# Kernel tuning notes

Measured on AMD Instinct MI355X. Metric: run time of the kernel, lower is better.

Reference implementation:

```python
import jax, jax.numpy as jnp
import numpy as np

D = 4          # subsample stride for quantized refs
R = 6          # local search radius
P = 2 * R + 1  # 13
N = P * P      # 169
C = 32         # one-hot classes
BETA = 50.0
SIG = 1.0      # gaussian kernel sigma for kernel_soft_argmax
MPR = 12       # memory_patch_R
MPP = 2 * MPR + 1  # 25
DIL_INT = 15


def bilinear_gather(img, ys, xs):
    # img (b,c,h,w); ys,xs (b,n,h,w) float pixel coords; zero padding outside.
    b, c, h, w = img.shape
    y0f = jnp.floor(ys); x0f = jnp.floor(xs)
    wy = ys - y0f; wx = xs - x0f
    y0 = y0f.astype(jnp.int32); x0 = x0f.astype(jnp.int32)
    imgf = img.reshape(b, c, h * w)

    def corner(yi, xi, wgt):
        valid = (yi >= 0) & (yi < h) & (xi >= 0) & (xi < w)
        idx = jnp.clip(yi, 0, h - 1) * w + jnp.clip(xi, 0, w - 1)  # (b,n,h,w)
        g = jax.vmap(lambda f, ix: f[:, ix])(imgf, idx)            # (b,c,n,h,w)
        return g * (wgt * valid)[:, None]

    return (corner(y0, x0, (1 - wy) * (1 - wx))
            + corner(y0, x0 + 1, (1 - wy) * wx)
            + corner(y0 + 1, x0, wy * (1 - wx))
            + corner(y0 + 1, x0 + 1, wy * wx))


def deform_im2col(img, offset):
    # img (b,c,h,w); offset (b,h,w,2) ordered (dx,dy); returns (b,c,N,h,w)
    b, c, h, w = img.shape
    n = jnp.arange(N)
    dy = (n // P - R).astype(jnp.float32)
    dx = (n % P - R).astype(jnp.float32)
    yy = jnp.arange(h, dtype=jnp.float32)[:, None]
    xx = jnp.arange(w, dtype=jnp.float32)[None, :]
    ys = yy[None, None] + offset[..., 1][:, None] + dy[None, :, None, None]
    xs = xx[None, None] + offset[..., 0][:, None] + dx[None, :, None, None]
    return bilinear_gather(img, ys, xs)


def local_corr(t, r, rad, dil):
    # SpatialCorrelationSampler(kernel_size=1, patch_size=2*rad+1, dilation_patch=dil)
    pad = rad * dil
    rp = jnp.pad(r, ((0, 0), (0, 0), (pad, pad), (pad, pad)))
    offs = jnp.arange(2 * rad + 1) * dil

    def dot(oy, ox):
        rs = jax.lax.dynamic_slice(rp, (0, 0, oy, ox), t.shape)
        return jnp.sum(t * rs, axis=1)  # (b,h,w)

    f = jax.vmap(lambda oy: jax.vmap(lambda ox: dot(oy, ox))(offs))(offs)  # (Pp,Pp,b,h,w)
    return jnp.transpose(f, (2, 0, 1, 3, 4))  # (b,Pp,Pp,h,w), axis1=dy, axis2=dx


def unfold(x, ksz, pad):
    # torch F.unfold: (b,c,h,w) -> (b,c,ksz*ksz,h*w), n = ky*ksz+kx, zero pad
    b, c, h, w = x.shape
    xp = jnp.pad(x, ((0, 0), (0, 0), (pad, pad), (pad, pad)))
    offs = jnp.arange(ksz)
    sl = jax.vmap(lambda oy: jax.vmap(
        lambda ox: jax.lax.dynamic_slice(xp, (0, 0, oy, ox), x.shape))(offs))(offs)
    return jnp.transpose(sl, (2, 3, 0, 1, 4, 5)).reshape(b, c, ksz * ksz, h * w)


def kernel_soft_argmax(corr):
    # corr (B, N, h, w): gaussian-weight then softmax(beta * .) over N
    k = jnp.arange(P, dtype=jnp.float32)
    ctr = (P - 1) / 2.0
    g = jnp.exp(-(((k[None, :] - ctr) ** 2) + ((k[:, None] - ctr) ** 2)) / (2 * SIG ** 2))
    return jax.nn.softmax(BETA * (g.reshape(1, N, 1, 1) * corr), axis=1)


def get_grid(corr):
    # corr (B, N, h, w) -> soft-argmax grid (B, h, w, 2) in normalized coords
    B, n, h, w = corr.shape
    # replicate the torch meshgrid variable swap in the original get_grid
    x_map = jnp.broadcast_to(jnp.linspace(-1.0, 1.0, w)[None, :], (h, w)).astype(jnp.float32)
    y_map = jnp.broadcast_to(jnp.linspace(-1.0, 1.0, h)[:, None], (h, w)).astype(jnp.float32)
    xg = unfold(x_map[None, None], P, R)[:, 0]  # (1,N,hw)
    yg = unfold(y_map[None, None], P, R)[:, 0]
    wgt = corr.reshape(B, n, h * w)
    wgt = wgt / jnp.sum(wgt, 1, keepdims=True)
    gx = (wgt * xg).sum(1).reshape(B, h, w, 1)
    gy = (wgt * yg).sum(1).reshape(B, h, w, 1)
    return jnp.concatenate([gx, gy], 3)


def forward(feats_r, feats_t, quantized_r, ref_index, current_ind):
    ref_list = [int(v) for v in np.asarray(ref_index)]  # static config
    cur = int(current_ind)
    nref = feats_r.shape[0]
    nsearch = len([x for x in ref_list if cur - x > DIL_INT])
    dirates = [min(4, (cur - x) // DIL_INT + 1) for x in ref_list if cur - x > DIL_INT]
    b, c, h, w = feats_t.shape

    mdy = jnp.arange(-MPR, MPR + 1, dtype=jnp.float32)
    corrs, offsets = [], []
    for si in range(nsearch):
        cc = local_corr(feats_t, feats_r[si], MPR, dirates[si])       # (b,25,25,h,w)
        cc = jax.nn.softmax(cc.reshape(b, MPP * MPP, h * w), axis=1)
        cc = cc.reshape(b, MPP, MPP, h, w)
        offx = jnp.einsum('bpqhw,q->bhw', cc, mdy)   # expectation of dx
        offy = jnp.einsum('bpqhw,p->bhw', cc, mdy)   # expectation of dy
        off = jnp.stack([offx, offy], -1) * float(dirates[si])        # (b,h,w,2)
        offsets.append(off)
        col0 = deform_im2col(feats_r[si], off)                        # (b,c,N,h,w)
        corrs.append(jnp.einsum('bchw,bcnhw->bnhw', feats_t, col0))
    for ind in range(nsearch, nref):
        corrs.append(local_corr(feats_t, feats_r[ind], R, 1).reshape(b, N, h, w))

    corr = jnp.concatenate(corrs, 0)                 # (b*nref, N, h, w)
    corr = kernel_soft_argmax(corr)
    corr = corr.reshape(b, 1, N * nref, h * w)
    grid = get_grid(corr.reshape(-1, N, h, w))       # (b*nref, h, w, 2)

    # prep: subsample ::D and one-hot single-channel label maps
    labels = quantized_r[:, :, 0, ::D, ::D]          # (nref, b, h, w)
    qr = (labels[:, :, None] == jnp.arange(C)[None, None, :, None, None]).astype(jnp.float32)

    cols = []
    for i in range(nsearch):
        cols.append(deform_im2col(qr[i], offsets[i]).reshape(b, C, N, h * w))
    for i in range(nsearch, nref):
        cols.append(unfold(qr[i], P, R))
    image_uf = jnp.concatenate(cols, 2)              # (b, C, N*nref, hw)

    out = jnp.einsum('bnl,bcnl->bcl', corr[:, 0], image_uf).reshape(b, C, h, w)
    return out, grid


def setup_inputs() -> dict:
    key = jax.random.key(0)
    k1, k2, k3 = jax.random.split(key, 3)
    feats_r = jax.random.normal(k1, (3, 1, 64, 64, 64), dtype=jnp.float32)
    feats_t = jax.random.normal(k2, (1, 64, 64, 64), dtype=jnp.float32)
    quantized_r = jax.random.randint(k3, (3, 1, 1, 256, 256), 0, C, dtype=jnp.int32)
    return {
        'feats_r': feats_r,
        'feats_t': feats_t,
        'quantized_r': quantized_r,
        'ref_index': np.arange(3),
        'current_ind': 16,
    }


def reference(feats_r, feats_t, quantized_r, ref_index, current_ind):
    return forward(feats_r, feats_t, quantized_r, ref_index, current_ind)
```

## Files before the change

kernel.cpp:

```cpp
#include <hip/hip_runtime.h>


#define NPIX 4096

__device__ __forceinline__ float pdot(float4 t0, float4 t1, float4 t2,
                                      float4 t3, float4 a, float4 b, float4 c,
                                      float4 d) {
  float s0 = 0.f, s1 = 0.f, s2 = 0.f, s3 = 0.f;
  s0 = fmaf(t0.x, a.x, s0); s1 = fmaf(t0.y, a.y, s1);
  s2 = fmaf(t0.z, a.z, s2); s3 = fmaf(t0.w, a.w, s3);
  s0 = fmaf(t1.x, b.x, s0); s1 = fmaf(t1.y, b.y, s1);
  s2 = fmaf(t1.z, b.z, s2); s3 = fmaf(t1.w, b.w, s3);
  s0 = fmaf(t2.x, c.x, s0); s1 = fmaf(t2.y, c.y, s1);
  s2 = fmaf(t2.z, c.z, s2); s3 = fmaf(t2.w, c.w, s3);
  s0 = fmaf(t3.x, d.x, s0); s1 = fmaf(t3.y, d.y, s1);
  s2 = fmaf(t3.z, d.z, s2); s3 = fmaf(t3.w, d.w, s3);
  return (s0 + s1) + (s2 + s3);
}

__device__ __forceinline__ float qdot(float4 ta, float4 tb, float4 tc,
                                      float4 td,
                                      const float* __restrict__ rbase,
                                      int tx) {
  const float4* r = (const float4*)rbase;
  float v = pdot(ta, tb, tc, td, r[tx], r[tx + 4], r[tx + 8], r[tx + 12]);
  v += __shfl_xor(v, 1);
  v += __shfl_xor(v, 2);
  return v;
}

__device__ __forceinline__ float xpose_reduce4(float p0, float p1, float p2,
                                               float p3, int tx) {
  bool o1 = tx & 1, o2 = tx & 2;
  float x01 = __shfl_xor(o1 ? p0 : p1, 1);
  float x23 = __shfl_xor(o1 ? p2 : p3, 1);
  float sA = (o1 ? p1 : p0) + x01;
  float sB = (o1 ? p3 : p2) + x23;
  float z = __shfl_xor(o2 ? sA : sB, 2);
  return o2 ? (sB + z) : (sA + z);
}

__global__ __launch_bounds__(256) void k_transpose(
    const float* __restrict__ ft, const float* __restrict__ fr,
    float* __restrict__ tT, float* __restrict__ rT) {
  __shared__ float tile[64][65];
  int img = blockIdx.y;
  int pixBase = blockIdx.x * 64;
  const float* src = (img == 0) ? ft : fr + (img - 1) * (64 * NPIX);
  float* dst = (img == 0) ? tT : rT + (img - 1) * (64 * NPIX);
  int tid = threadIdx.x;
#pragma unroll
  for (int it = 0; it < 16; ++it) {
    int li = it * 256 + tid;
    int c = li >> 6, p = li & 63;
    tile[p][c] = src[c * NPIX + pixBase + p];
  }
  __syncthreads();
#pragma unroll
  for (int it = 0; it < 16; ++it) {
    int li = it * 256 + tid;
    int p = li >> 6, c = li & 63;
    dst[(pixBase + p) * 64 + c] = tile[p][c];
  }
}

#define LOADT(N, XC)                                                       \
  const float4* tp##N = (const float4*)&tT[((y << 6) + (XC)) << 6];        \
  float4 t##N##0 = tp##N[tx], t##N##1 = tp##N[tx + 4],                     \
         t##N##2 = tp##N[tx + 8], t##N##3 = tp##N[tx + 12];

__global__ __launch_bounds__(256) void k_corr_all(
    const float* __restrict__ tT, const float* __restrict__ rT,
    float* __restrict__ off, float* __restrict__ corrws,
    float* __restrict__ grid) {
  int z = blockIdx.z;
  int xg = blockIdx.x, y = blockIdx.y;
  int tid = threadIdx.x;
  int g = tid >> 2, tx = tid & 3;
  int w = tid >> 6, lane = tid & 63;
  __shared__ float cc[4][625];
  __shared__ float offs[4][2];

  if (z == 0) {
    int x0 = (xg >> 1) * 8 + (xg & 1);
    LOADT(0, x0 + 0) LOADT(1, x0 + 2) LOADT(2, x0 + 4) LOADT(3, x0 + 6)

#pragma unroll 2
    for (int r = 0; r < 11; ++r) {
      int tu = g + (r << 6);
      if (tu < 700) {
        int oy = tu / 28, u = tu - oy * 28;
        int ry = y + 2 * (oy - 12), rx = x0 - 24 + 2 * u;
        float4 ra, rb, rc, rd;
        if ((unsigned)ry < 64u && (unsigned)rx < 64u) {
          const float4* rp = (const float4*)&rT[(ry * 64 + rx) * 64];
          ra = rp[tx]; rb = rp[tx + 4]; rc = rp[tx + 8]; rd = rp[tx + 12];
        } else {
          ra = rb = rc = rd = make_float4(0.f, 0.f, 0.f, 0.f);
        }
        float p0 = pdot(t00, t01, t02, t03, ra, rb, rc, rd);
        float p1 = pdot(t10, t11, t12, t13, ra, rb, rc, rd);
        float p2 = pdot(t20, t21, t22, t23, ra, rb, rc, rd);
        float p3 = pdot(t30, t31, t32, t33, ra, rb, rc, rd);
        float v = xpose_reduce4(p0, p1, p2, p3, tx);
        int ox = u - tx;
        if ((unsigned)ox < 25u) cc[tx][oy * 25 + ox] = v;
      }
    }
    __syncthreads();

    {
      float vv[10];
      float lmax = -3e38f;
#pragma unroll
      for (int it = 0; it < 10; ++it) {
        int o = lane + it * 64;
        float v = (o < 625) ? cc[w][o] : -3e38f;
        vv[it] = v;
        lmax = fmaxf(lmax, v);
      }
#pragma unroll
      for (int o = 32; o; o >>= 1) lmax = fmaxf(lmax, __shfl_down(lmax, o));
      float m = __shfl(lmax, 0);
      float s = 0.f, sx = 0.f, sy = 0.f;
#pragma unroll
      for (int it = 0; it < 10; ++it) {
        int o = lane + it * 64;
        int oy = o / 25, ox = o - oy * 25;
        float e = __expf(vv[it] - m);
        s += e;
        sx += e * (float)(ox - 12);
        sy += e * (float)(oy - 12);
      }
#pragma unroll
      for (int o = 32; o; o >>= 1) {
        s += __shfl_down(s, o);
        sx += __shfl_down(sx, o);
        sy += __shfl_down(sy, o);
      }
      if (lane == 0) {
        float ox_ = 2.f * sx / s, oy_ = 2.f * sy / s;
        offs[w][0] = ox_;
        offs[w][1] = oy_;
        int pix = y * 64 + x0 + 2 * w;
        off[pix * 2 + 0] = ox_;
        off[pix * 2 + 1] = oy_;
      }
    }
    __syncthreads();

    float(*D)[196] = (float(*)[196]) & cc[0][0];
#pragma unroll 1
    for (int r = 0; r < 13; ++r) {
      int s3 = g + (r << 6);
      if (s3 < 784) {
        int p = s3 / 196;
        int idx = s3 - p * 196;
        int a = idx / 14, b2 = idx - a * 14;
        float offx = offs[p][0], offy = offs[p][1];
        int px = x0 + 2 * p;
        int iy0 = y + (int)floorf(offy), ix0 = px + (int)floorf(offx);
        int ry = iy0 - 6 + a, rx = ix0 - 6 + b2;
        float v = 0.f;
        if ((unsigned)ry < 64u && (unsigned)rx < 64u) {
          const float4* tq = (const float4*)&tT[(y * 64 + px) * 64];
          v = qdot(tq[tx], tq[tx + 4], tq[tx + 8], tq[tx + 12],
                   &rT[(ry * 64 + rx) * 64], tx);
        }
        if (tx == 0) D[p][idx] = v;
      }
    }
    __syncthreads();

    {
      int px = x0 + 2 * w;
      int pix = y * 64 + px;
      float offx = offs[w][0], offy = offs[w][1];
      float fy = floorf(offy), fx = floorf(offx);
      float wy = offy - fy, wx = offx - fx;
      float w00 = (1.f - wy) * (1.f - wx), w01 = (1.f - wy) * wx;
      float w10 = wy * (1.f - wx), w11 = wy * wx;
      float sc[3];
      float lmax = -3e38f;
#pragma unroll
      for (int it = 0; it < 3; ++it) {
        int o = lane + it * 64;
        float scv = -3e38f;
        if (o < 169) {
          int i = o / 13, j = o - i * 13;
          float v = w00 * D[w][i * 14 + j] + w01 * D[w][i * 14 + j + 1] +
                    w10 * D[w][(i + 1) * 14 + j] +
                    w11 * D[w][(i + 1) * 14 + j + 1];
          float di = (float)((i - 6) * (i - 6) + (j - 6) * (j - 6));
          scv = 50.f * __expf(-0.5f * di) * v;
        }
        sc[it] = scv;
        lmax = fmaxf(lmax, scv);
      }
#pragma unroll
      for (int o = 32; o; o >>= 1) lmax = fmaxf(lmax, __shfl_down(lmax, o));
      float m = __shfl(lmax, 0);
      float ee[3];
      float s = 0.f, gx = 0.f, gy = 0.f;
#pragma unroll
      for (int it = 0; it < 3; ++it) {
        int o = lane + it * 64;
        int i = o / 13, j = o - i * 13;
        float e = __expf(sc[it] - m);
        ee[it] = e;
        int yy = y + i - 6, xx = px + j - 6;
        bool inb = (o < 169) && (unsigned)yy < 64u && (unsigned)xx < 64u;
        float xgv = inb ? (-1.f + (2.f / 63.f) * (float)xx) : 0.f;
        float ygv = inb ? (-1.f + (2.f / 63.f) * (float)yy) : 0.f;
        s += e;
        gx += e * xgv;
        gy += e * ygv;
      }
#pragma unroll
      for (int o = 32; o; o >>= 1) {
        s += __shfl_down(s, o);
        gx += __shfl_down(gx, o);
        gy += __shfl_down(gy, o);
      }
      float S = __shfl(s, 0);
#pragma unroll
      for (int it = 0; it < 3; ++it) {
        int o = lane + it * 64;
        if (o < 169) corrws[pix * 169 + o] = ee[it] / S;
      }
      if (lane == 0) {
        grid[pix * 2 + 0] = gx / S;
        grid[pix * 2 + 1] = gy / S;
      }
    }
  } else {
    int k = z;
    int x0 = xg * 4;
    const float* rb0 = rT + k * (64 * NPIX);
    LOADT(0, x0 + 0) LOADT(1, x0 + 1) LOADT(2, x0 + 2) LOADT(3, x0 + 3)
    float(*cc2)[169] = (float(*)[169]) & cc[0][0];

#pragma unroll 2
    for (int r = 0; r < 4; ++r) {
      int tu = g + (r << 6);
      if (tu < 208) {
        int i = tu >> 4, u = tu & 15;
        int ry = y + i - 6, rx = x0 - 6 + u;
        float4 ra, rbv, rc, rd;
        if ((unsigned)ry < 64u && (unsigned)rx < 64u) {
          const float4* rp = (const float4*)&rb0[(ry * 64 + rx) * 64];
          ra = rp[tx]; rbv = rp[tx + 4]; rc = rp[tx + 8]; rd = rp[tx + 12];
        } else {
          ra = rbv = rc = rd = make_float4(0.f, 0.f, 0.f, 0.f);
        }
        float p0 = pdot(t00, t01, t02, t03, ra, rbv, rc, rd);
        float p1 = pdot(t10, t11, t12, t13, ra, rbv, rc, rd);
        float p2 = pdot(t20, t21, t22, t23, ra, rbv, rc, rd);
        float p3 = pdot(t30, t31, t32, t33, ra, rbv, rc, rd);
        float v = xpose_reduce4(p0, p1, p2, p3, tx);
        int j = u - tx;
        if ((unsigned)j < 13u) cc2[tx][i * 13 + j] = v;
      }
    }
    __syncthreads();

    int px = x0 + w;
    int pix = y * 64 + px;
    float sc[3];
    float lmax = -3e38f;
#pragma unroll
    for (int it = 0; it < 3; ++it) {
      int o = lane + it * 64;
      float scv = -3e38f;
      if (o < 169) {
        int i = o / 13, j = o - i * 13;
        float di = (float)((i - 6) * (i - 6) + (j - 6) * (j - 6));
        scv = 50.f * __expf(-0.5f * di) * cc2[w][o];
      }
      sc[it] = scv;
      lmax = fmaxf(lmax, scv);
    }
#pragma unroll
    for (int o = 32; o; o >>= 1) lmax = fmaxf(lmax, __shfl_down(lmax, o));
    float m = __shfl(lmax, 0);
    float ee[3];
    float s = 0.f, gx = 0.f, gy = 0.f;
#pragma unroll
    for (int it = 0; it < 3; ++it) {
      int o = lane + it * 64;
      int i = o / 13, j = o - i * 13;
      float e = __expf(sc[it] - m);
      ee[it] = e;
      int yy = y + i - 6, xx = px + j - 6;
      bool inb = (o < 169) && (unsigned)yy < 64u && (unsigned)xx < 64u;
      float xgv = inb ? (-1.f + (2.f / 63.f) * (float)xx) : 0.f;
      float ygv = inb ? (-1.f + (2.f / 63.f) * (float)yy) : 0.f;
      s += e;
      gx += e * xgv;
      gy += e * ygv;
    }
#pragma unroll
    for (int o = 32; o; o >>= 1) {
      s += __shfl_down(s, o);
      gx += __shfl_down(gx, o);
      gy += __shfl_down(gy, o);
    }
    float S = __shfl(s, 0);
#pragma unroll
    for (int it = 0; it < 3; ++it) {
      int o = lane + it * 64;
      if (o < 169) corrws[(k * NPIX + pix) * 169 + o] = ee[it] / S;
    }
    if (lane == 0) {
      grid[(k * NPIX + pix) * 2 + 0] = gx / S;
      grid[(k * NPIX + pix) * 2 + 1] = gy / S;
    }
  }
}

__global__ __launch_bounds__(256) void k_out(const float* __restrict__ corrws,
                                             const float* __restrict__ off,
                                             const int* __restrict__ q,
                                             float* __restrict__ out) {
  int tid = threadIdx.x;
  int pix0 = blockIdx.x * 8;
  __shared__ float bins[8][32];
  __shared__ float cr[8][169];
  __shared__ float offs[8][2];
  bins[tid >> 5][tid & 31] = 0.f;
  if (tid < 16) offs[tid >> 1][tid & 1] = off[(pix0 + (tid >> 1)) * 2 + (tid & 1)];
  for (int i = tid; i < 8 * 169; i += 256) {
    int g = i / 169, n = i - g * 169;
    cr[g][n] = corrws[(pix0 + g) * 169 + n];
  }
  __syncthreads();

  for (int s = tid; s < 8 * 196; s += 256) {
    int g = s / 196, m = s - g * 196;
    int a = m / 14, b = m - a * 14;
    int pix = pix0 + g, y = pix >> 6, x = pix & 63;
    float offx = offs[g][0], offy = offs[g][1];
    float fy = floorf(offy), fx = floorf(offx);
    float wy = offy - fy, wx = offx - fx;
    int ry = y + (int)fy - 6 + a, rx = x + (int)fx - 6 + b;
    if ((unsigned)ry < 64u && (unsigned)rx < 64u) {
      float w00 = (1.f - wy) * (1.f - wx), w01 = (1.f - wy) * wx;
      float w10 = wy * (1.f - wx), w11 = wy * wx;
      float wgt = 0.f;
      if (a < 13) {
        if (b < 13) wgt = fmaf(w00, cr[g][a * 13 + b], wgt);
        if (b > 0) wgt = fmaf(w01, cr[g][a * 13 + b - 1], wgt);
      }
      if (a > 0) {
        if (b < 13) wgt = fmaf(w10, cr[g][(a - 1) * 13 + b], wgt);
        if (b > 0) wgt = fmaf(w11, cr[g][(a - 1) * 13 + b - 1], wgt);
      }
      if (wgt != 0.f) {
        int lbl = q[ry * 1024 + rx * 4];
        atomicAdd(&bins[g][lbl], wgt);
      }
    }
  }

  for (int k = 1; k < 3; ++k) {
    __syncthreads();
    for (int i = tid; i < 8 * 169; i += 256) {
      int g = i / 169, n = i - g * 169;
      cr[g][n] = corrws[((k << 12) + pix0 + g) * 169 + n];
    }
    __syncthreads();
    for (int s = tid; s < 8 * 169; s += 256) {
      int g = s / 169, n = s - g * 169;
      int i2 = n / 13, j2 = n - i2 * 13;
      int pix = pix0 + g, y = pix >> 6, x = pix & 63;
      int yy = y + i2 - 6, xx = x + j2 - 6;
      if ((unsigned)yy < 64u && (unsigned)xx < 64u) {
        int lbl = q[k * 65536 + yy * 1024 + xx * 4];
        atomicAdd(&bins[g][lbl], cr[g][n]);
      }
    }
  }
  __syncthreads();
  out[(tid >> 3) * NPIX + pix0 + (tid & 7)] = bins[tid & 7][tid >> 3];
}

extern "C" void kernel_launch(void* const* d_in, const int* in_sizes, int n_in,
                              void* d_out, int out_size, void* d_ws,
                              size_t ws_size, hipStream_t stream) {
  const float* fr = (const float*)d_in[0];
  const float* ft = (const float*)d_in[1];
  const int* q = (const int*)d_in[2];
  float* out = (float*)d_out;
  float* grid = out + 32 * NPIX;

  float* ws = (float*)d_ws;
  float* tT = ws;
  float* rT = ws + 262144;
  float* off = ws + 1048576;
  float* corrws = ws + 1056768;

  k_transpose<<<dim3(64, 4), 256, 0, stream>>>(ft, fr, tT, rT);
  k_corr_all<<<dim3(16, 64, 3), 256, 0, stream>>>(tT, rT, off, corrws, grid);
  k_out<<<512, 256, 0, stream>>>(corrws, off, q, out);
}
```

Before: 61.44 us.

## Pack subsampled labels to bytes, restructure correlation loops with clamped branchless loads

The transpose kernel now also writes the subsampled labels as a compact byte array. k_out copies all three reference label planes into shared memory and maps threads to a fixed 2D (a,b) window per pixel, which removes divisions and strided global label reads. The correlation phases replace divide/modulo indexing and per-thread branches with fixed row/column assignments, clamped loads and masked results. Phase 3 reuses the target registers already loaded instead of reloading them. Each k_out block now loads 12KB of labels, which adds redundant traffic and shared-memory pressure.

```diff
diff --git a/kernel.cpp b/kernel.cpp
--- a/kernel.cpp
+++ b/kernel.cpp
@@ -18,17 +18,6 @@
   return (s0 + s1) + (s2 + s3);
 }
 
-__device__ __forceinline__ float qdot(float4 ta, float4 tb, float4 tc,
-                                      float4 td,
-                                      const float* __restrict__ rbase,
-                                      int tx) {
-  const float4* r = (const float4*)rbase;
-  float v = pdot(ta, tb, tc, td, r[tx], r[tx + 4], r[tx + 8], r[tx + 12]);
-  v += __shfl_xor(v, 1);
-  v += __shfl_xor(v, 2);
-  return v;
-}
-
 __device__ __forceinline__ float xpose_reduce4(float p0, float p1, float p2,
                                                float p3, int tx) {
   bool o1 = tx & 1, o2 = tx & 2;
@@ -42,7 +31,8 @@
 
 __global__ __launch_bounds__(256) void k_transpose(
     const float* __restrict__ ft, const float* __restrict__ fr,
-    float* __restrict__ tT, float* __restrict__ rT) {
+    const int* __restrict__ q, float* __restrict__ tT, float* __restrict__ rT,
+    unsigned char* __restrict__ lblp) {
   __shared__ float tile[64][65];
   int img = blockIdx.y;
   int pixBase = blockIdx.x * 64;
@@ -62,12 +52,37 @@
     int p = li >> 6, c = li & 63;
     dst[(pixBase + p) * 64 + c] = tile[p][c];
   }
+  if (img >= 1 && tid < 64) {
+    int pix = pixBase + tid;
+    lblp[(img - 1) * 4096 + pix] =
+        (unsigned char)q[(img - 1) * 65536 + (pix >> 6) * 1024 + (pix & 63) * 4];
+  }
 }
 
 #define LOADT(N, XC)                                                       \
   const float4* tp##N = (const float4*)&tT[((y << 6) + (XC)) << 6];        \
   float4 t##N##0 = tp##N[tx], t##N##1 = tp##N[tx + 4],                     \
          t##N##2 = tp##N[tx + 8], t##N##3 = tp##N[tx + 12];
+
+__device__ __forceinline__ void phase3_px(
+    float4 T0, float4 T1, float4 T2, float4 T3, int iy0, int ix0,
+    const float* __restrict__ rT, float* __restrict__ Dp, int aB, int b3,
+    int tx) {
+#pragma unroll 1
+  for (int r = 0; r < 4; ++r) {
+    int a = aB + 4 * r;
+    int ry = iy0 + a, rx = ix0 + b3;
+    bool ok = (a < 14) & (b3 < 14) & ((unsigned)ry < 64u) & ((unsigned)rx < 64u);
+    int ryc = min(max(ry, 0), 63), rxc = min(max(rx, 0), 63);
+    const float4* rp = (const float4*)&rT[(ryc * 64 + rxc) * 64 + tx * 4];
+    float4 ra = rp[0], rb = rp[4], rc = rp[8], rd = rp[12];
+    float v = pdot(T0, T1, T2, T3, ra, rb, rc, rd);
+    v += __shfl_xor(v, 1);
+    v += __shfl_xor(v, 2);
+    v = ok ? v : 0.f;
+    if ((a < 14) && (b3 < 14) && tx == 0) Dp[a * 14 + b3] = v;
+  }
+}
 
 __global__ __launch_bounds__(256) void k_corr_all(
     const float* __restrict__ tT, const float* __restrict__ rT,
@@ -85,26 +100,32 @@
     int x0 = (xg >> 1) * 8 + (xg & 1);
     LOADT(0, x0 + 0) LOADT(1, x0 + 2) LOADT(2, x0 + 4) LOADT(3, x0 + 6)
 
-#pragma unroll 2
-    for (int r = 0; r < 11; ++r) {
-      int tu = g + (r << 6);
-      if (tu < 700) {
-        int oy = tu / 28, u = tu - oy * 28;
-        int ry = y + 2 * (oy - 12), rx = x0 - 24 + 2 * u;
-        float4 ra, rb, rc, rd;
-        if ((unsigned)ry < 64u && (unsigned)rx < 64u) {
-          const float4* rp = (const float4*)&rT[(ry * 64 + rx) * 64];
-          ra = rp[tx]; rb = rp[tx + 4]; rc = rp[tx + 8]; rd = rp[tx + 12];
-        } else {
-          ra = rb = rc = rd = make_float4(0.f, 0.f, 0.f, 0.f);
-        }
+    {
+      int u = g & 31;
+      int rx = x0 - 24 + 2 * u;
+      bool col_ok = ((unsigned)rx < 64u) & (u < 28);
+      int rx_c = min(max(rx, 0), 63);
+      int colB = rx_c * 64 + tx * 4;
+      int ox = u - tx;
+      bool st_col = (unsigned)ox < 25u;
+      int oy = g >> 5;
+      int ry = y + 2 * oy - 24;
+#pragma unroll 1
+      for (int r = 0; r < 13; ++r) {
+        bool oy_ok = oy < 25;
+        bool ok = col_ok & oy_ok & ((unsigned)ry < 64u);
+        int ry_c = min(max(ry, 0), 63);
+        const float4* rp = (const float4*)&rT[ry_c * 4096 + colB];
+        float4 ra = rp[0], rb = rp[4], rc = rp[8], rd = rp[12];
         float p0 = pdot(t00, t01, t02, t03, ra, rb, rc, rd);
         float p1 = pdot(t10, t11, t12, t13, ra, rb, rc, rd);
         float p2 = pdot(t20, t21, t22, t23, ra, rb, rc, rd);
         float p3 = pdot(t30, t31, t32, t33, ra, rb, rc, rd);
         float v = xpose_reduce4(p0, p1, p2, p3, tx);
-        int ox = u - tx;
-        if ((unsigned)ox < 25u) cc[tx][oy * 25 + ox] = v;
+        v = ok ? v : 0.f;
+        if (st_col && oy_ok) cc[tx][oy * 25 + ox] = v;
+        oy += 2;
+        ry += 4;
       }
     }
     __syncthreads();
@@ -150,24 +171,27 @@
     __syncthreads();
 
     float(*D)[196] = (float(*)[196]) & cc[0][0];
-#pragma unroll 1
-    for (int r = 0; r < 13; ++r) {
-      int s3 = g + (r << 6);
-      if (s3 < 784) {
-        int p = s3 / 196;
-        int idx = s3 - p * 196;
-        int a = idx / 14, b2 = idx - a * 14;
-        float offx = offs[p][0], offy = offs[p][1];
-        int px = x0 + 2 * p;
-        int iy0 = y + (int)floorf(offy), ix0 = px + (int)floorf(offx);
-        int ry = iy0 - 6 + a, rx = ix0 - 6 + b2;
-        float v = 0.f;
-        if ((unsigned)ry < 64u && (unsigned)rx < 64u) {
-          const float4* tq = (const float4*)&tT[(y * 64 + px) * 64];
-          v = qdot(tq[tx], tq[tx + 4], tq[tx + 8], tq[tx + 12],
-                   &rT[(ry * 64 + rx) * 64], tx);
-        }
-        if (tx == 0) D[p][idx] = v;
+    {
+      int b3 = g & 15, aB = g >> 4;
+      {
+        float offx = offs[0][0], offy = offs[0][1];
+        phase3_px(t00, t01, t02, t03, y + (int)floorf(offy) - 6,
+                  x0 + 0 + (int)floorf(offx) - 6, rT, &D[0][0], aB, b3, tx);
+      }
+      {
+        float offx = offs[1][0], offy = offs[1][1];
+        phase3_px(t10, t11, t12, t13, y + (int)floorf(offy) - 6,
+                  x0 + 2 + (int)floorf(offx) - 6, rT, &D[1][0], aB, b3, tx);
+      }
+      {
+        float offx = offs[2][0], offy = offs[2][1];
+        phase3_px(t20, t21, t22, t23, y + (int)floorf(offy) - 6,
+                  x0 + 4 + (int)floorf(offx) - 6, rT, &D[2][0], aB, b3, tx);
+      }
+      {
+        float offx = offs[3][0], offy = offs[3][1];
+        phase3_px(t30, t31, t32, t33, y + (int)floorf(offy) - 6,
+                  x0 + 6 + (int)floorf(offx) - 6, rT, &D[3][0], aB, b3, tx);
       }
     }
     __syncthreads();
@@ -240,26 +264,32 @@
     LOADT(0, x0 + 0) LOADT(1, x0 + 1) LOADT(2, x0 + 2) LOADT(3, x0 + 3)
     float(*cc2)[169] = (float(*)[169]) & cc[0][0];
 
-#pragma unroll 2
-    for (int r = 0; r < 4; ++r) {
-      int tu = g + (r << 6);
-      if (tu < 208) {
-        int i = tu >> 4, u = tu & 15;
-        int ry = y + i - 6, rx = x0 - 6 + u;
-        float4 ra, rbv, rc, rd;
-        if ((unsigned)ry < 64u && (unsigned)rx < 64u) {
-          const float4* rp = (const float4*)&rb0[(ry * 64 + rx) * 64];
-          ra = rp[tx]; rbv = rp[tx + 4]; rc = rp[tx + 8]; rd = rp[tx + 12];
-        } else {
-          ra = rbv = rc = rd = make_float4(0.f, 0.f, 0.f, 0.f);
-        }
+    {
+      int u2 = g & 15;
+      int rx = x0 - 6 + u2;
+      bool col_ok = (unsigned)rx < 64u;
+      int rx_c = min(max(rx, 0), 63);
+      int colB = rx_c * 64 + tx * 4;
+      int j = u2 - tx;
+      bool st_col = (unsigned)j < 13u;
+      int i = g >> 4;
+      int ry = y + i - 6;
+#pragma unroll 1
+      for (int r = 0; r < 4; ++r) {
+        bool i_ok = i < 13;
+        bool ok = col_ok & i_ok & ((unsigned)ry < 64u);
+        int ry_c = min(max(ry, 0), 63);
+        const float4* rp = (const float4*)&rb0[ry_c * 4096 + colB];
+        float4 ra = rp[0], rbv = rp[4], rc = rp[8], rd = rp[12];
         float p0 = pdot(t00, t01, t02, t03, ra, rbv, rc, rd);
         float p1 = pdot(t10, t11, t12, t13, ra, rbv, rc, rd);
         float p2 = pdot(t20, t21, t22, t23, ra, rbv, rc, rd);
         float p3 = pdot(t30, t31, t32, t33, ra, rbv, rc, rd);
         float v = xpose_reduce4(p0, p1, p2, p3, tx);
-        int j = u - tx;
-        if ((unsigned)j < 13u) cc2[tx][i * 13 + j] = v;
+        v = ok ? v : 0.f;
+        if (st_col && i_ok) cc2[tx][i * 13 + j] = v;
+        i += 4;
+        ry += 4;
       }
     }
     __syncthreads();
@@ -318,65 +348,81 @@
   }
 }
 
-__global__ __launch_bounds__(256) void k_out(const float* __restrict__ corrws,
-                                             const float* __restrict__ off,
-                                             const int* __restrict__ q,
-                                             float* __restrict__ out) {
+__global__ __launch_bounds__(256) void k_out(
+    const float* __restrict__ corrws, const float* __restrict__ off,
+    const unsigned char* __restrict__ lblp, float* __restrict__ out) {
   int tid = threadIdx.x;
   int pix0 = blockIdx.x * 8;
-  __shared__ float bins[8][32];
+  __shared__ float bins[8][33];
   __shared__ float cr[8][169];
-  __shared__ float offs[8][2];
-  bins[tid >> 5][tid & 31] = 0.f;
-  if (tid < 16) offs[tid >> 1][tid & 1] = off[(pix0 + (tid >> 1)) * 2 + (tid & 1)];
-  for (int i = tid; i < 8 * 169; i += 256) {
-    int g = i / 169, n = i - g * 169;
-    cr[g][n] = corrws[(pix0 + g) * 169 + n];
-  }
-  __syncthreads();
-
-  for (int s = tid; s < 8 * 196; s += 256) {
-    int g = s / 196, m = s - g * 196;
-    int a = m / 14, b = m - a * 14;
-    int pix = pix0 + g, y = pix >> 6, x = pix & 63;
-    float offx = offs[g][0], offy = offs[g][1];
+  __shared__ __align__(16) unsigned char lbl[3 * 4096];
+  __shared__ float w4[8][4];
+  __shared__ int bse[8][2];
+
+  for (int i = tid; i < 264; i += 256) ((float*)bins)[i] = 0.f;
+  for (int i = tid; i < 768; i += 256)
+    ((int4*)lbl)[i] = ((const int4*)lblp)[i];
+  for (int i = tid; i < 1352; i += 256) {
+    int g2 = i / 169, n = i - g2 * 169;
+    cr[g2][n] = corrws[(pix0 + g2) * 169 + n];
+  }
+  if (tid < 8) {
+    float offx = off[(pix0 + tid) * 2 + 0], offy = off[(pix0 + tid) * 2 + 1];
     float fy = floorf(offy), fx = floorf(offx);
     float wy = offy - fy, wx = offx - fx;
-    int ry = y + (int)fy - 6 + a, rx = x + (int)fx - 6 + b;
-    if ((unsigned)ry < 64u && (unsigned)rx < 64u) {
-      float w00 = (1.f - wy) * (1.f - wx), w01 = (1.f - wy) * wx;
-      float w10 = wy * (1.f - wx), w11 = wy * wx;
-      float wgt = 0.f;
-      if (a < 13) {
-        if (b < 13) wgt = fmaf(w00, cr[g][a * 13 + b], wgt);
-        if (b > 0) wgt = fmaf(w01, cr[g][a * 13 + b - 1], wgt);
-      }
-      if (a > 0) {
-        if (b < 13) wgt = fmaf(w10, cr[g][(a - 1) * 13 + b], wgt);
-        if (b > 0) wgt = fmaf(w11, cr[g][(a - 1) * 13 + b - 1], wgt);
-      }
-      if (wgt != 0.f) {
-        int lbl = q[ry * 1024 + rx * 4];
-        atomicAdd(&bins[g][lbl], wgt);
-      }
-    }
-  }
-
-  for (int k = 1; k < 3; ++k) {
-    __syncthreads();
-    for (int i = tid; i < 8 * 169; i += 256) {
-      int g = i / 169, n = i - g * 169;
-      cr[g][n] = corrws[((k << 12) + pix0 + g) * 169 + n];
-    }
-    __syncthreads();
-    for (int s = tid; s < 8 * 169; s += 256) {
-      int g = s / 169, n = s - g * 169;
-      int i2 = n / 13, j2 = n - i2 * 13;
-      int pix = pix0 + g, y = pix >> 6, x = pix & 63;
-      int yy = y + i2 - 6, xx = x + j2 - 6;
-      if ((unsigned)yy < 64u && (unsigned)xx < 64u) {
-        int lbl = q[k * 65536 + yy * 1024 + xx * 4];
-        atomicAdd(&bins[g][lbl], cr[g][n]);
+    w4[tid][0] = (1.f - wy) * (1.f - wx);
+    w4[tid][1] = (1.f - wy) * wx;
+    w4[tid][2] = wy * (1.f - wx);
+    w4[tid][3] = wy * wx;
+    int pix = pix0 + tid;
+    bse[tid][0] = (pix >> 6) + (int)fy - 6;
+    bse[tid][1] = (pix & 63) + (int)fx - 6;
+  }
+  __syncthreads();
+
+  {
+    int a = tid >> 4, b = tid & 15;
+    bool act0 = (tid < 224) && (b < 14);
+#pragma unroll 1
+    for (int p = 0; p < 8; ++p) {
+      if (act0) {
+        int ry = bse[p][0] + a, rx = bse[p][1] + b;
+        if ((unsigned)ry < 64u && (unsigned)rx < 64u) {
+          float wgt = 0.f;
+          const float* crp = cr[p];
+          if (a < 13) {
+            if (b < 13) wgt = fmaf(w4[p][0], crp[a * 13 + b], wgt);
+            if (b > 0) wgt = fmaf(w4[p][1], crp[a * 13 + b - 1], wgt);
+          }
+          if (a > 0) {
+            if (b < 13) wgt = fmaf(w4[p][2], crp[(a - 1) * 13 + b], wgt);
+            if (b > 0) wgt = fmaf(w4[p][3], crp[(a - 1) * 13 + b - 1], wgt);
+          }
+          if (wgt != 0.f) atomicAdd(&bins[p][lbl[ry * 64 + rx]], wgt);
+        }
+      }
+    }
+  }
+
+  {
+    int i2 = tid >> 4, j2 = tid & 15;
+    bool act12 = (tid < 208) && (j2 < 13);
+    for (int k = 1; k < 3; ++k) {
+      __syncthreads();
+      for (int i = tid; i < 1352; i += 256) {
+        int g2 = i / 169, n = i - g2 * 169;
+        cr[g2][n] = corrws[((k << 12) + pix0 + g2) * 169 + n];
+      }
+      __syncthreads();
+#pragma unroll 1
+      for (int p = 0; p < 8; ++p) {
+        if (act12) {
+          int pix = pix0 + p;
+          int yy = (pix >> 6) + i2 - 6, xx = (pix & 63) + j2 - 6;
+          if ((unsigned)yy < 64u && (unsigned)xx < 64u)
+            atomicAdd(&bins[p][lbl[(k << 12) + yy * 64 + xx]],
+                      cr[p][i2 * 13 + j2]);
+        }
       }
     }
   }
@@ -398,8 +444,9 @@
   float* rT = ws + 262144;
   float* off = ws + 1048576;
   float* corrws = ws + 1056768;
-
-  k_transpose<<<dim3(64, 4), 256, 0, stream>>>(ft, fr, tT, rT);
+  unsigned char* lblp = (unsigned char*)(ws + 3133440);
+
+  k_transpose<<<dim3(64, 4), 256, 0, stream>>>(ft, fr, q, tT, rT, lblp);
   k_corr_all<<<dim3(16, 64, 3), 256, 0, stream>>>(tT, rT, off, corrws, grid);
-  k_out<<<512, 256, 0, stream>>>(corrws, off, q, out);
-}
+  k_out<<<512, 256, 0, stream>>>(corrws, off, lblp, out);
+}
```

Result: no change. 60.69 us (-1.2%).

## Fuse correlation, softmax and label binning into one kernel per pixel group

Applied to the files above, without the earlier changes.

Merges the per-reference correlation blocks and the output-binning kernel into a single kernel. Each block now handles four pixels across all three references and accumulates label bins in shared memory, so the corrws and offset workspace round-trips and the third launch go away. The transpose kernel is vectorized with float4 and also packs the subsampled labels into a byte array. The first-stage loop is restructured to prefetch rows with clamped addresses instead of branching. In exchange there are fewer blocks (1024 instead of 3072) and more serialized work per block, which may reduce parallelism.

```diff
diff --git a/kernel.cpp b/kernel.cpp
--- a/kernel.cpp
+++ b/kernel.cpp
@@ -42,7 +42,8 @@
 
 __global__ __launch_bounds__(256) void k_transpose(
     const float* __restrict__ ft, const float* __restrict__ fr,
-    float* __restrict__ tT, float* __restrict__ rT) {
+    const int* __restrict__ q, float* __restrict__ tT, float* __restrict__ rT,
+    unsigned char* __restrict__ lblp) {
   __shared__ float tile[64][65];
   int img = blockIdx.y;
   int pixBase = blockIdx.x * 64;
@@ -50,17 +51,30 @@
   float* dst = (img == 0) ? tT : rT + (img - 1) * (64 * NPIX);
   int tid = threadIdx.x;
 #pragma unroll
-  for (int it = 0; it < 16; ++it) {
-    int li = it * 256 + tid;
-    int c = li >> 6, p = li & 63;
-    tile[p][c] = src[c * NPIX + pixBase + p];
-  }
-  __syncthreads();
-#pragma unroll
-  for (int it = 0; it < 16; ++it) {
-    int li = it * 256 + tid;
-    int p = li >> 6, c = li & 63;
-    dst[(pixBase + p) * 64 + c] = tile[p][c];
+  for (int it = 0; it < 4; ++it) {
+    int idx = it * 256 + tid;
+    int c = idx >> 4;
+    int p4 = (idx & 15) << 2;
+    float4 v = *(const float4*)&src[c * NPIX + pixBase + p4];
+    tile[p4 + 0][c] = v.x;
+    tile[p4 + 1][c] = v.y;
+    tile[p4 + 2][c] = v.z;
+    tile[p4 + 3][c] = v.w;
+  }
+  __syncthreads();
+#pragma unroll
+  for (int it = 0; it < 4; ++it) {
+    int idx = it * 256 + tid;
+    int p = idx >> 4;
+    int c4 = (idx & 15) << 2;
+    float4 v = make_float4(tile[p][c4], tile[p][c4 + 1], tile[p][c4 + 2],
+                           tile[p][c4 + 3]);
+    *(float4*)&dst[(pixBase + p) * 64 + c4] = v;
+  }
+  if (img >= 1 && tid < 64) {
+    int pix = pixBase + tid;
+    lblp[(img - 1) * 4096 + pix] = (unsigned char)
+        q[(img - 1) * 65536 + (pix >> 6) * 1024 + (pix & 63) * 4];
   }
 }
 
@@ -69,117 +83,235 @@
   float4 t##N##0 = tp##N[tx], t##N##1 = tp##N[tx + 4],                     \
          t##N##2 = tp##N[tx + 8], t##N##3 = tp##N[tx + 12];
 
-__global__ __launch_bounds__(256) void k_corr_all(
+#define PH3(P, T0, T1, T2, T3)                                             \
+  {                                                                        \
+    float offx = offs[P][0], offy = offs[P][1];                            \
+    int iy0 = y + (int)floorf(offy) - 6;                                   \
+    int ix0 = x0 + 2 * (P) + (int)floorf(offx) - 6;                        \
+    _Pragma("unroll 2") for (int r = 0; r < 4; ++r) {                      \
+      int s = g + (r << 6);                                                \
+      int a = s / 14, b = s - a * 14;                                      \
+      int ry = iy0 + a, rx = ix0 + b;                                      \
+      bool ok = (s < 196) & ((unsigned)ry < 64u) & ((unsigned)rx < 64u);   \
+      int ryc = min(max(ry, 0), 63), rxc = min(max(rx, 0), 63);            \
+      float v = qdot(T0, T1, T2, T3, &rT[(ryc * 64 + rxc) * 64], tx);      \
+      v = ok ? v : 0.f;                                                    \
+      if ((s < 196) && tx == 0) ccf[(P) * 196 + s] = v;                    \
+    }                                                                      \
+  }
+
+__global__ __launch_bounds__(256) void k_fused(
     const float* __restrict__ tT, const float* __restrict__ rT,
-    float* __restrict__ off, float* __restrict__ corrws,
+    const unsigned char* __restrict__ lblp, float* __restrict__ out,
     float* __restrict__ grid) {
-  int z = blockIdx.z;
   int xg = blockIdx.x, y = blockIdx.y;
+  int x0 = (xg >> 1) * 8 + (xg & 1);
   int tid = threadIdx.x;
   int g = tid >> 2, tx = tid & 3;
   int w = tid >> 6, lane = tid & 63;
-  __shared__ float cc[4][625];
+  __shared__ float ccf[2500];
   __shared__ float offs[4][2];
-
-  if (z == 0) {
-    int x0 = (xg >> 1) * 8 + (xg & 1);
-    LOADT(0, x0 + 0) LOADT(1, x0 + 2) LOADT(2, x0 + 4) LOADT(3, x0 + 6)
-
+  __shared__ float bins[4][33];
+
+  if (tid < 132) ((float*)bins)[tid] = 0.f;
+
+  LOADT(0, x0 + 0) LOADT(1, x0 + 2) LOADT(2, x0 + 4) LOADT(3, x0 + 6)
+
+  {
+    int u = g & 31;
+    int rx = x0 - 24 + 2 * u;
+    bool col_ok = ((unsigned)rx < 64u) & (u < 28);
+    int rx_c = min(max(rx, 0), 63);
+    int colB = rx_c * 64 + tx * 4;
+    int ox = u - tx;
+    bool st_col = (unsigned)ox < 25u;
+    int oy = g >> 5;
+    int ry = y + 2 * oy - 24;
+    int ry_c = min(max(ry, 0), 63);
+    const float4* rp = (const float4*)&rT[ry_c * 4096 + colB];
+    float4 ra = rp[0], rb = rp[4], rc = rp[8], rd = rp[12];
+#pragma unroll 1
+    for (int r = 0; r < 13; ++r) {
+      int ry_n = ry + 4;
+      int ryn_c = min(max(ry_n, 0), 63);
+      const float4* np = (const float4*)&rT[ryn_c * 4096 + colB];
+      float4 na = np[0], nb = np[4], nc = np[8], nd = np[12];
+      float p0 = pdot(t00, t01, t02, t03, ra, rb, rc, rd);
+      float p1 = pdot(t10, t11, t12, t13, ra, rb, rc, rd);
+      float p2 = pdot(t20, t21, t22, t23, ra, rb, rc, rd);
+      float p3 = pdot(t30, t31, t32, t33, ra, rb, rc, rd);
+      float v = xpose_reduce4(p0, p1, p2, p3, tx);
+      bool ok = col_ok & (oy < 25) & ((unsigned)ry < 64u);
+      v = ok ? v : 0.f;
+      if (st_col && (oy < 25)) ccf[tx * 625 + oy * 25 + ox] = v;
+      oy += 2;
+      ry = ry_n;
+      ra = na; rb = nb; rc = nc; rd = nd;
+    }
+  }
+  __syncthreads();
+
+  {
+    float vv[10];
+    float lmax = -3e38f;
+#pragma unroll
+    for (int it = 0; it < 10; ++it) {
+      int o = lane + it * 64;
+      float v = (o < 625) ? ccf[w * 625 + o] : -3e38f;
+      vv[it] = v;
+      lmax = fmaxf(lmax, v);
+    }
+#pragma unroll
+    for (int o = 32; o; o >>= 1) lmax = fmaxf(lmax, __shfl_down(lmax, o));
+    float m = __shfl(lmax, 0);
+    float s = 0.f, sx = 0.f, sy = 0.f;
+#pragma unroll
+    for (int it = 0; it < 10; ++it) {
+      int o = lane + it * 64;
+      int oy = o / 25, ox = o - oy * 25;
+      float e = __expf(vv[it] - m);
+      s += e;
+      sx += e * (float)(ox - 12);
+      sy += e * (float)(oy - 12);
+    }
+#pragma unroll
+    for (int o = 32; o; o >>= 1) {
+      s += __shfl_down(s, o);
+      sx += __shfl_down(sx, o);
+      sy += __shfl_down(sy, o);
+    }
+    if (lane == 0) {
+      offs[w][0] = 2.f * sx / s;
+      offs[w][1] = 2.f * sy / s;
+    }
+  }
+  __syncthreads();
+
+  PH3(0, t00, t01, t02, t03)
+  PH3(1, t10, t11, t12, t13)
+  PH3(2, t20, t21, t22, t23)
+  PH3(3, t30, t31, t32, t33)
+  __syncthreads();
+
+  {
+    int px = x0 + 2 * w;
+    int pix = y * 64 + px;
+    float offx = offs[w][0], offy = offs[w][1];
+    float fy = floorf(offy), fx = floorf(offx);
+    float wy = offy - fy, wx = offx - fx;
+    float w00 = (1.f - wy) * (1.f - wx), w01 = (1.f - wy) * wx;
+    float w10 = wy * (1.f - wx), w11 = wy * wx;
+    const float* Dw = &ccf[w * 196];
+    float sc[3];
+    float lmax = -3e38f;
+#pragma unroll
+    for (int it = 0; it < 3; ++it) {
+      int o = lane + it * 64;
+      float scv = -3e38f;
+      if (o < 169) {
+        int i = o / 13, j = o - i * 13;
+        float v = w00 * Dw[i * 14 + j] + w01 * Dw[i * 14 + j + 1] +
+                  w10 * Dw[(i + 1) * 14 + j] + w11 * Dw[(i + 1) * 14 + j + 1];
+        float di = (float)((i - 6) * (i - 6) + (j - 6) * (j - 6));
+        scv = 50.f * __expf(-0.5f * di) * v;
+      }
+      sc[it] = scv;
+      lmax = fmaxf(lmax, scv);
+    }
+#pragma unroll
+    for (int o = 32; o; o >>= 1) lmax = fmaxf(lmax, __shfl_down(lmax, o));
+    float m = __shfl(lmax, 0);
+    float ee[3];
+    float s = 0.f, gx = 0.f, gy = 0.f;
+#pragma unroll
+    for (int it = 0; it < 3; ++it) {
+      int o = lane + it * 64;
+      int i = o / 13, j = o - i * 13;
+      float e = __expf(sc[it] - m);
+      ee[it] = e;
+      int yy = y + i - 6, xx = px + j - 6;
+      bool inb = (o < 169) && (unsigned)yy < 64u && (unsigned)xx < 64u;
+      float xgv = inb ? (-1.f + (2.f / 63.f) * (float)xx) : 0.f;
+      float ygv = inb ? (-1.f + (2.f / 63.f) * (float)yy) : 0.f;
+      s += e;
+      gx += e * xgv;
+      gy += e * ygv;
+    }
+#pragma unroll
+    for (int o = 32; o; o >>= 1) {
+      s += __shfl_down(s, o);
+      gx += __shfl_down(gx, o);
+      gy += __shfl_down(gy, o);
+    }
+    float S = __shfl(s, 0);
+    float invS = 1.f / S;
+#pragma unroll
+    for (int it = 0; it < 3; ++it) {
+      int o = lane + it * 64;
+      if (o < 169) ccf[1024 + w * 169 + o] = ee[it] * invS;
+    }
+    if (lane == 0) {
+      grid[pix * 2 + 0] = gx * invS;
+      grid[pix * 2 + 1] = gy * invS;
+    }
+  }
+  __syncthreads();
+
+  {
+#pragma unroll 1
+    for (int s = tid; s < 784; s += 256) {
+      int p = s / 196, m2 = s - p * 196;
+      int a = m2 / 14, b = m2 - a * 14;
+      float offx = offs[p][0], offy = offs[p][1];
+      float fy = floorf(offy), fx = floorf(offx);
+      float wy = offy - fy, wx = offx - fx;
+      int ry = y + (int)fy - 6 + a;
+      int rx = x0 + 2 * p + (int)fx - 6 + b;
+      if ((unsigned)ry < 64u && (unsigned)rx < 64u) {
+        float w00 = (1.f - wy) * (1.f - wx), w01 = (1.f - wy) * wx;
+        float w10 = wy * (1.f - wx), w11 = wy * wx;
+        const float* crp = &ccf[1024 + p * 169];
+        float wgt = 0.f;
+        if (a < 13) {
+          if (b < 13) wgt = fmaf(w00, crp[a * 13 + b], wgt);
+          if (b > 0) wgt = fmaf(w01, crp[a * 13 + b - 1], wgt);
+        }
+        if (a > 0) {
+          if (b < 13) wgt = fmaf(w10, crp[(a - 1) * 13 + b], wgt);
+          if (b > 0) wgt = fmaf(w11, crp[(a - 1) * 13 + b - 1], wgt);
+        }
+        if (wgt != 0.f) atomicAdd(&bins[p][lblp[ry * 64 + rx]], wgt);
+      }
+    }
+  }
+
+  for (int k = 1; k <= 2; ++k) {
+    __syncthreads();
+    const float* rb0 = rT + k * (64 * NPIX);
+    {
 #pragma unroll 2
-    for (int r = 0; r < 11; ++r) {
-      int tu = g + (r << 6);
-      if (tu < 700) {
-        int oy = tu / 28, u = tu - oy * 28;
-        int ry = y + 2 * (oy - 12), rx = x0 - 24 + 2 * u;
-        float4 ra, rb, rc, rd;
-        if ((unsigned)ry < 64u && (unsigned)rx < 64u) {
-          const float4* rp = (const float4*)&rT[(ry * 64 + rx) * 64];
-          ra = rp[tx]; rb = rp[tx + 4]; rc = rp[tx + 8]; rd = rp[tx + 12];
-        } else {
-          ra = rb = rc = rd = make_float4(0.f, 0.f, 0.f, 0.f);
-        }
+      for (int r = 0; r < 4; ++r) {
+        int tu = g + (r << 6);
+        int i = tu / 19, u = tu - i * 19;
+        int ry = y + i - 6, rx = x0 - 6 + u;
+        bool ok = (i < 13) & ((unsigned)ry < 64u) & ((unsigned)rx < 64u);
+        int ryc = min(max(ry, 0), 63), rxc = min(max(rx, 0), 63);
+        const float4* rp = (const float4*)&rb0[(ryc * 64 + rxc) * 64 + tx * 4];
+        float4 ra = rp[0], rb = rp[4], rc = rp[8], rd = rp[12];
         float p0 = pdot(t00, t01, t02, t03, ra, rb, rc, rd);
         float p1 = pdot(t10, t11, t12, t13, ra, rb, rc, rd);
         float p2 = pdot(t20, t21, t22, t23, ra, rb, rc, rd);
         float p3 = pdot(t30, t31, t32, t33, ra, rb, rc, rd);
         float v = xpose_reduce4(p0, p1, p2, p3, tx);
-        int ox = u - tx;
-        if ((unsigned)ox < 25u) cc[tx][oy * 25 + ox] = v;
+        v = ok ? v : 0.f;
+        int j = u - 2 * tx;
+        if ((i < 13) && ((unsigned)j < 13u)) ccf[tx * 169 + i * 13 + j] = v;
       }
     }
     __syncthreads();
-
-    {
-      float vv[10];
-      float lmax = -3e38f;
-#pragma unroll
-      for (int it = 0; it < 10; ++it) {
-        int o = lane + it * 64;
-        float v = (o < 625) ? cc[w][o] : -3e38f;
-        vv[it] = v;
-        lmax = fmaxf(lmax, v);
-      }
-#pragma unroll
-      for (int o = 32; o; o >>= 1) lmax = fmaxf(lmax, __shfl_down(lmax, o));
-      float m = __shfl(lmax, 0);
-      float s = 0.f, sx = 0.f, sy = 0.f;
-#pragma unroll
-      for (int it = 0; it < 10; ++it) {
-        int o = lane + it * 64;
-        int oy = o / 25, ox = o - oy * 25;
-        float e = __expf(vv[it] - m);
-        s += e;
-        sx += e * (float)(ox - 12);
-        sy += e * (float)(oy - 12);
-      }
-#pragma unroll
-      for (int o = 32; o; o >>= 1) {
-        s += __shfl_down(s, o);
-        sx += __shfl_down(sx, o);
-        sy += __shfl_down(sy, o);
-      }
-      if (lane == 0) {
-        float ox_ = 2.f * sx / s, oy_ = 2.f * sy / s;
-        offs[w][0] = ox_;
-        offs[w][1] = oy_;
-        int pix = y * 64 + x0 + 2 * w;
-        off[pix * 2 + 0] = ox_;
-        off[pix * 2 + 1] = oy_;
-      }
-    }
-    __syncthreads();
-
-    float(*D)[196] = (float(*)[196]) & cc[0][0];
-#pragma unroll 1
-    for (int r = 0; r < 13; ++r) {
-      int s3 = g + (r << 6);
-      if (s3 < 784) {
-        int p = s3 / 196;
-        int idx = s3 - p * 196;
-        int a = idx / 14, b2 = idx - a * 14;
-        float offx = offs[p][0], offy = offs[p][1];
-        int px = x0 + 2 * p;
-        int iy0 = y + (int)floorf(offy), ix0 = px + (int)floorf(offx);
-        int ry = iy0 - 6 + a, rx = ix0 - 6 + b2;
-        float v = 0.f;
-        if ((unsigned)ry < 64u && (unsigned)rx < 64u) {
-          const float4* tq = (const float4*)&tT[(y * 64 + px) * 64];
-          v = qdot(tq[tx], tq[tx + 4], tq[tx + 8], tq[tx + 12],
-                   &rT[(ry * 64 + rx) * 64], tx);
-        }
-        if (tx == 0) D[p][idx] = v;
-      }
-    }
-    __syncthreads();
-
     {
       int px = x0 + 2 * w;
       int pix = y * 64 + px;
-      float offx = offs[w][0], offy = offs[w][1];
-      float fy = floorf(offy), fx = floorf(offx);
-      float wy = offy - fy, wx = offx - fx;
-      float w00 = (1.f - wy) * (1.f - wx), w01 = (1.f - wy) * wx;
-      float w10 = wy * (1.f - wx), w11 = wy * wx;
       float sc[3];
       float lmax = -3e38f;
 #pragma unroll
@@ -188,11 +320,8 @@
         float scv = -3e38f;
         if (o < 169) {
           int i = o / 13, j = o - i * 13;
-          float v = w00 * D[w][i * 14 + j] + w01 * D[w][i * 14 + j + 1] +
-                    w10 * D[w][(i + 1) * 14 + j] +
-                    w11 * D[w][(i + 1) * 14 + j + 1];
           float di = (float)((i - 6) * (i - 6) + (j - 6) * (j - 6));
-          scv = 50.f * __expf(-0.5f * di) * v;
+          scv = 50.f * __expf(-0.5f * di) * ccf[w * 169 + o];
         }
         sc[it] = scv;
         lmax = fmaxf(lmax, scv);
@@ -223,165 +352,30 @@
         gy += __shfl_down(gy, o);
       }
       float S = __shfl(s, 0);
+      float invS = 1.f / S;
 #pragma unroll
       for (int it = 0; it < 3; ++it) {
         int o = lane + it * 64;
-        if (o < 169) corrws[pix * 169 + o] = ee[it] / S;
+        if (o < 169) {
+          int i = o / 13, j = o - i * 13;
+          int yy = y + i - 6, xx = px + j - 6;
+          if ((unsigned)yy < 64u && (unsigned)xx < 64u)
+            atomicAdd(&bins[w][lblp[(k << 12) + yy * 64 + xx]],
+                      ee[it] * invS);
+        }
       }
       if (lane == 0) {
-        grid[pix * 2 + 0] = gx / S;
-        grid[pix * 2 + 1] = gy / S;
-      }
-    }
-  } else {
-    int k = z;
-    int x0 = xg * 4;
-    const float* rb0 = rT + k * (64 * NPIX);
-    LOADT(0, x0 + 0) LOADT(1, x0 + 1) LOADT(2, x0 + 2) LOADT(3, x0 + 3)
-    float(*cc2)[169] = (float(*)[169]) & cc[0][0];
-
-#pragma unroll 2
-    for (int r = 0; r < 4; ++r) {
-      int tu = g + (r << 6);
-      if (tu < 208) {
-        int i = tu >> 4, u = tu & 15;
-        int ry = y + i - 6, rx = x0 - 6 + u;
-        float4 ra, rbv, rc, rd;
-        if ((unsigned)ry < 64u && (unsigned)rx < 64u) {
-          const float4* rp = (const float4*)&rb0[(ry * 64 + rx) * 64];
-          ra = rp[tx]; rbv = rp[tx + 4]; rc = rp[tx + 8]; rd = rp[tx + 12];
-        } else {
-          ra = rbv = rc = rd = make_float4(0.f, 0.f, 0.f, 0.f);
-        }
-        float p0 = pdot(t00, t01, t02, t03, ra, rbv, rc, rd);
-        float p1 = pdot(t10, t11, t12, t13, ra, rbv, rc, rd);
-        float p2 = pdot(t20, t21, t22, t23, ra, rbv, rc, rd);
-        float p3 = pdot(t30, t31, t32, t33, ra, rbv, rc, rd);
-        float v = xpose_reduce4(p0, p1, p2, p3, tx);
-        int j = u - tx;
-        if ((unsigned)j < 13u) cc2[tx][i * 13 + j] = v;
-      }
-    }
-    __syncthreads();
-
-    int px = x0 + w;
-    int pix = y * 64 + px;
-    float sc[3];
-    float lmax = -3e38f;
-#pragma unroll
-    for (int it = 0; it < 3; ++it) {
-      int o = lane + it * 64;
-      float scv = -3e38f;
-      if (o < 169) {
-        int i = o / 13, j = o - i * 13;
-        float di = (float)((i - 6) * (i - 6) + (j - 6) * (j - 6));
-        scv = 50.f * __expf(-0.5f * di) * cc2[w][o];
-      }
-      sc[it] = scv;
-      lmax = fmaxf(lmax, scv);
-    }
-#pragma unroll
-    for (int o = 32; o; o >>= 1) lmax = fmaxf(lmax, __shfl_down(lmax, o));
-    float m = __shfl(lmax, 0);
-    float ee[3];
-    float s = 0.f, gx = 0.f, gy = 0.f;
-#pragma unroll
-    for (int it = 0; it < 3; ++it) {
-      int o = lane + it * 64;
-      int i = o / 13, j = o - i * 13;
-      float e = __expf(sc[it] - m);
-      ee[it] = e;
-      int yy = y + i - 6, xx = px + j - 6;
-      bool inb = (o < 169) && (unsigned)yy < 64u && (unsigned)xx < 64u;
-      float xgv = inb ? (-1.f + (2.f / 63.f) * (float)xx) : 0.f;
-      float ygv = inb ? (-1.f + (2.f / 63.f) * (float)yy) : 0.f;
-      s += e;
-      gx += e * xgv;
-      gy += e * ygv;
-    }
-#pragma unroll
-    for (int o = 32; o; o >>= 1) {
-      s += __shfl_down(s, o);
-      gx += __shfl_down(gx, o);
-      gy += __shfl_down(gy, o);
-    }
-    float S = __shfl(s, 0);
-#pragma unroll
-    for (int it = 0; it < 3; ++it) {
-      int o = lane + it * 64;
-      if (o < 169) corrws[(k * NPIX + pix) * 169 + o] = ee[it] / S;
-    }
-    if (lane == 0) {
-      grid[(k * NPIX + pix) * 2 + 0] = gx / S;
-      grid[(k * NPIX + pix) * 2 + 1] = gy / S;
-    }
-  }
-}
-
-__global__ __launch_bounds__(256) void k_out(const float* __restrict__ corrws,
-                                             const float* __restrict__ off,
-                                             const int* __restrict__ q,
-                                             float* __restrict__ out) {
-  int tid = threadIdx.x;
-  int pix0 = blockIdx.x * 8;
-  __shared__ float bins[8][32];
-  __shared__ float cr[8][169];
-  __shared__ float offs[8][2];
-  bins[tid >> 5][tid & 31] = 0.f;
-  if (tid < 16) offs[tid >> 1][tid & 1] = off[(pix0 + (tid >> 1)) * 2 + (tid & 1)];
-  for (int i = tid; i < 8 * 169; i += 256) {
-    int g = i / 169, n = i - g * 169;
-    cr[g][n] = corrws[(pix0 + g) * 169 + n];
-  }
-  __syncthreads();
-
-  for (int s = tid; s < 8 * 196; s += 256) {
-    int g = s / 196, m = s - g * 196;
-    int a = m / 14, b = m - a * 14;
-    int pix = pix0 + g, y = pix >> 6, x = pix & 63;
-    float offx = offs[g][0], offy = offs[g][1];
-    float fy = floorf(offy), fx = floorf(offx);
-    float wy = offy - fy, wx = offx - fx;
-    int ry = y + (int)fy - 6 + a, rx = x + (int)fx - 6 + b;
-    if ((unsigned)ry < 64u && (unsigned)rx < 64u) {
-      float w00 = (1.f - wy) * (1.f - wx), w01 = (1.f - wy) * wx;
-      float w10 = wy * (1.f - wx), w11 = wy * wx;
-      float wgt = 0.f;
-      if (a < 13) {
-        if (b < 13) wgt = fmaf(w00, cr[g][a * 13 + b], wgt);
-        if (b > 0) wgt = fmaf(w01, cr[g][a * 13 + b - 1], wgt);
-      }
-      if (a > 0) {
-        if (b < 13) wgt = fmaf(w10, cr[g][(a - 1) * 13 + b], wgt);
-        if (b > 0) wgt = fmaf(w11, cr[g][(a - 1) * 13 + b - 1], wgt);
-      }
-      if (wgt != 0.f) {
-        int lbl = q[ry * 1024 + rx * 4];
-        atomicAdd(&bins[g][lbl], wgt);
-      }
-    }
-  }
-
-  for (int k = 1; k < 3; ++k) {
-    __syncthreads();
-    for (int i = tid; i < 8 * 169; i += 256) {
-      int g = i / 169, n = i - g * 169;
-      cr[g][n] = corrws[((k << 12) + pix0 + g) * 169 + n];
-    }
-    __syncthreads();
-    for (int s = tid; s < 8 * 169; s += 256) {
-      int g = s / 169, n = s - g * 169;
-      int i2 = n / 13, j2 = n - i2 * 13;
-      int pix = pix0 + g, y = pix >> 6, x = pix & 63;
-      int yy = y + i2 - 6, xx = x + j2 - 6;
-      if ((unsigned)yy < 64u && (unsigned)xx < 64u) {
-        int lbl = q[k * 65536 + yy * 1024 + xx * 4];
-        atomicAdd(&bins[g][lbl], cr[g][n]);
-      }
-    }
-  }
-  __syncthreads();
-  out[(tid >> 3) * NPIX + pix0 + (tid & 7)] = bins[tid & 7][tid >> 3];
+        grid[(k * NPIX + pix) * 2 + 0] = gx * invS;
+        grid[(k * NPIX + pix) * 2 + 1] = gy * invS;
+      }
+    }
+  }
+  __syncthreads();
+
+  if (tid < 128) {
+    int p = tid & 3, c = tid >> 2;
+    out[c * NPIX + y * 64 + x0 + 2 * p] = bins[p][c];
+  }
 }
 
 extern "C" void kernel_launch(void* const* d_in, const int* in_sizes, int n_in,
@@ -396,10 +390,8 @@
   float* ws = (float*)d_ws;
   float* tT = ws;
   float* rT = ws + 262144;
-  float* off = ws + 1048576;
-  float* corrws = ws + 1056768;
-
-  k_transpose<<<dim3(64, 4), 256, 0, stream>>>(ft, fr, tT, rT);
-  k_corr_all<<<dim3(16, 64, 3), 256, 0, stream>>>(tT, rT, off, corrws, grid);
-  k_out<<<512, 256, 0, stream>>>(corrws, off, q, out);
-}
+  unsigned char* lblp = (unsigned char*)(ws + 1048576);
+
+  k_transpose<<<dim3(64, 4), 256, 0, stream>>>(ft, fr, q, tT, rT, lblp);
+  k_fused<<<dim3(16, 64), 256, 0, stream>>>(tT, rT, lblp, out, grid);
+}
```

After: 58.96 us. 1.04x faster.
